# Kernel tuning notes

Hardware: AMD Instinct MI355X
Metric: run time of the kernel (lower is better)

The kernel has to match this reference:

```python
import jax, jax.numpy as jnp
import numpy as np
from jax import lax

VOCAB, EMB, HID = 50000, 1024, 1024
H2 = HID // 2            # per-direction LSTM hidden
T = 4096                 # sequence length
NTAGS, START, STOP = 5, 3, 4
NEG = -10000.0


def setup_inputs() -> dict:
    key = jax.random.key(0)
    ks = jax.random.split(key, 16)
    n = lambda i, shape, s=0.05: (jax.random.normal(ks[i], shape) * s).astype(jnp.float32)
    inp = {
        "sentence": jax.random.randint(ks[0], (T,), 0, VOCAB, dtype=jnp.int64 if jax.config.jax_enable_x64 else jnp.int32),
        "h0": jax.random.normal(ks[1], (2, H2), jnp.float32),
        "c0": jax.random.normal(ks[2], (2, H2), jnp.float32),
        "embed": jax.random.normal(ks[3], (VOCAB, EMB), jnp.float32),
        "Wih_f": n(4, (4 * H2, EMB)), "Whh_f": n(5, (4 * H2, H2)),
        "bih_f": n(6, (4 * H2,)),     "bhh_f": n(7, (4 * H2,)),
        "Wih_b": n(8, (4 * H2, EMB)), "Whh_b": n(9, (4 * H2, H2)),
        "bih_b": n(10, (4 * H2,)),    "bhh_b": n(11, (4 * H2,)),
        "Wout": n(12, (NTAGS, HID)),  "bout": n(13, (NTAGS,)),
    }
    trans = jax.random.normal(ks[14], (NTAGS, NTAGS), jnp.float32)
    trans = trans.at[START, :].set(NEG).at[:, STOP].set(NEG)
    inp["trans"] = trans
    return inp


def _lstm_dir(xs, h0, c0, Wih, Whh, bih, bhh):
    # torch LSTM gate order: i, f, g, o
    def step(carry, x):
        h, c = carry
        g = Wih @ x + bih + Whh @ h + bhh
        i, f, gg, o = jnp.split(g, 4)
        c = jax.nn.sigmoid(f) * c + jax.nn.sigmoid(i) * jnp.tanh(gg)
        h = jax.nn.sigmoid(o) * jnp.tanh(c)
        return (h, c), h
    _, hs = lax.scan(step, (h0, c0), xs)
    return hs  # [T, H2]


def reference(sentence, h0, c0, embed,
              Wih_f, Whh_f, bih_f, bhh_f,
              Wih_b, Whh_b, bih_b, bhh_b,
              Wout, bout, trans):
    xs = embed[sentence]  # [T, EMB]
    hf = _lstm_dir(xs, h0[0], c0[0], Wih_f, Whh_f, bih_f, bhh_f)
    hb = _lstm_dir(xs[::-1], h0[1], c0[1], Wih_b, Whh_b, bih_b, bhh_b)[::-1]
    feats = jnp.concatenate([hf, hb], axis=-1) @ Wout.T + bout  # [T, NTAGS]

    # Viterbi decode
    fv0 = jnp.full((NTAGS,), NEG, jnp.float32).at[START].set(0.0)

    def vstep(fv, feat):
        scores = fv[None, :] + trans            # [next_tag, prev_tag]
        bp = jnp.argmax(scores, axis=1)         # best prev for each next
        fv_new = jnp.max(scores, axis=1) + feat
        return fv_new, bp

    fv, bptrs = lax.scan(vstep, fv0, feats)     # bptrs: [T, NTAGS]
    terminal = fv + trans[STOP]
    best = jnp.argmax(terminal)
    path_score = terminal[best]

    def back(tag, bp):
        prev = bp[tag]
        return prev, prev
    _, path_rev = lax.scan(back, best, bptrs[::-1])  # tags at t=T-1..0, last is START
    full = jnp.concatenate([best[None], path_rev])    # length T+1
    best_path = full[::-1][1:]                        # drop START, forward order, length T
    return path_score, best_path
```

## Files before the change

kernel.cpp:

```cpp
#include <hip/hip_runtime.h>
#include <math.h>

#define VOCAB 50000
#define EMB   1024
#define H2    512
#define R4    2048
#define TLEN  4096
#define NTAGS 5
#define STARTT 3
#define STOPT  4
#define NEGV  (-10000.0f)

#define DWG   32
#define SLICE 16

typedef unsigned long long u64;

#define ALOAD64(p)    __hip_atomic_load((p), __ATOMIC_RELAXED, __HIP_MEMORY_SCOPE_AGENT)
#define ASTORE64(p,v) __hip_atomic_store((p), (v), __ATOMIC_RELAXED, __HIP_MEMORY_SCOPE_AGENT)

__device__ __forceinline__ float fsig(float x) {
    return __builtin_amdgcn_rcpf(1.f + __expf(-x));
}
__device__ __forceinline__ float ftanh(float x) {
    return 1.f - 2.f * __builtin_amdgcn_rcpf(1.f + __expf(2.f * x));
}

__global__ __launch_bounds__(256) void input_gemm(
    const int* __restrict__ sent, const float* __restrict__ embed,
    const float* __restrict__ WihF, const float* __restrict__ WihB,
    const float* __restrict__ bihF, const float* __restrict__ bhhF,
    const float* __restrict__ bihB, const float* __restrict__ bhhB,
    float* __restrict__ G)
{
    __shared__ float As[32 * 64];
    __shared__ float Bs[32 * 64];
    const int tid = threadIdx.x;
    const int tm = blockIdx.x * 64;
    const int tn = blockIdx.y * 64;
    const int dir = blockIdx.z;
    const float* Wih = dir ? WihB : WihF;

    const int lr = tid >> 2;
    const int lp = tid & 3;
    const int srow = sent[tm + lr];
    const float* arow = embed + (size_t)srow * EMB;
    const float* brow = Wih + (size_t)(tn + lr) * EMB;

    const int mt = (tid & 15) * 4;
    const int nt = (tid >> 4) * 4;
    float acc[4][4] = {};

    for (int k0 = 0; k0 < EMB; k0 += 32) {
        float4 a0 = *(const float4*)(arow + k0 + lp * 8);
        float4 a1 = *(const float4*)(arow + k0 + lp * 8 + 4);
        float4 b0 = *(const float4*)(brow + k0 + lp * 8);
        float4 b1 = *(const float4*)(brow + k0 + lp * 8 + 4);
        __syncthreads();
        const int kb = lp * 8;
        As[(kb + 0) * 64 + lr] = a0.x; As[(kb + 1) * 64 + lr] = a0.y;
        As[(kb + 2) * 64 + lr] = a0.z; As[(kb + 3) * 64 + lr] = a0.w;
        As[(kb + 4) * 64 + lr] = a1.x; As[(kb + 5) * 64 + lr] = a1.y;
        As[(kb + 6) * 64 + lr] = a1.z; As[(kb + 7) * 64 + lr] = a1.w;
        Bs[(kb + 0) * 64 + lr] = b0.x; Bs[(kb + 1) * 64 + lr] = b0.y;
        Bs[(kb + 2) * 64 + lr] = b0.z; Bs[(kb + 3) * 64 + lr] = b0.w;
        Bs[(kb + 4) * 64 + lr] = b1.x; Bs[(kb + 5) * 64 + lr] = b1.y;
        Bs[(kb + 6) * 64 + lr] = b1.z; Bs[(kb + 7) * 64 + lr] = b1.w;
        __syncthreads();
        #pragma unroll
        for (int k = 0; k < 32; ++k) {
            float4 av = *(const float4*)(As + k * 64 + mt);
            float4 bv = *(const float4*)(Bs + k * 64 + nt);
            acc[0][0] += av.x * bv.x; acc[0][1] += av.x * bv.y; acc[0][2] += av.x * bv.z; acc[0][3] += av.x * bv.w;
            acc[1][0] += av.y * bv.x; acc[1][1] += av.y * bv.y; acc[1][2] += av.y * bv.z; acc[1][3] += av.y * bv.w;
            acc[2][0] += av.z * bv.x; acc[2][1] += av.z * bv.y; acc[2][2] += av.z * bv.z; acc[2][3] += av.z * bv.w;
            acc[3][0] += av.w * bv.x; acc[3][1] += av.w * bv.y; acc[3][2] += av.w * bv.z; acc[3][3] += av.w * bv.w;
        }
    }

    const float* bih = dir ? bihB : bihF;
    const float* bhh = dir ? bhhB : bhhF;
    float4 bias;
    bias.x = bih[tn + nt + 0] + bhh[tn + nt + 0];
    bias.y = bih[tn + nt + 1] + bhh[tn + nt + 1];
    bias.z = bih[tn + nt + 2] + bhh[tn + nt + 2];
    bias.w = bih[tn + nt + 3] + bhh[tn + nt + 3];
    float* Gd = G + (size_t)dir * TLEN * R4;
    #pragma unroll
    for (int ii = 0; ii < 4; ++ii) {
        float4 o;
        o.x = acc[ii][0] + bias.x; o.y = acc[ii][1] + bias.y;
        o.z = acc[ii][2] + bias.z; o.w = acc[ii][3] + bias.w;
        *(float4*)(Gd + (size_t)(tm + mt + ii) * R4 + tn + nt) = o;
    }
}

__global__ __launch_bounds__(256, 1) void lstm_rec(
    const float* __restrict__ WhhF, const float* __restrict__ WhhB,
    const float* __restrict__ h0, const float* __restrict__ c0,
    const float* __restrict__ G, float* __restrict__ hs,
    u64* hbuf)
{
    const int tid  = threadIdx.x;
    const int dir  = blockIdx.x >> 5;
    const int wg   = blockIdx.x & 31;
    const int base = wg * SLICE;
    const int wave = tid >> 6;
    const int wl   = tid & 63;
    const int e_loc = wl >> 4;
    const int gp    = (wl >> 3) & 1;
    const int qs    = wl & 7;
    const int e     = wave * 4 + e_loc;
    const int grow0 = gp * H2 + base + e;
    const int grow1 = (gp + 2) * H2 + base + e;
    const bool prod = (wl & 15) == 0;
    const float* Whh = dir ? WhhB : WhhF;

    float4 W0[16], W1[16];
    {
        const float4* s0 = (const float4*)(Whh + (size_t)grow0 * H2 + qs * 64);
        const float4* s1 = (const float4*)(Whh + (size_t)grow1 * H2 + qs * 64);
        #pragma unroll
        for (int j = 0; j < 16; ++j) { W0[j] = s0[j]; W1[j] = s1[j]; }
    }

    __shared__ float hsh[8 * 68];

    u64* hb = hbuf + (size_t)dir * 2 * H2;
    float cc = 0.f;
    if (prod) {
        cc = c0[dir * H2 + base + e];
        float hv = h0[dir * H2 + base + e];
        u64 pack = ((u64)1u << 32) | (u64)__float_as_uint(hv);
        ASTORE64(hb + base + e, pack);
    }

    const float* Gd = G + (size_t)dir * TLEN * R4;
    float* hsd = hs + (size_t)dir * TLEN * H2;

    for (int s = 0; s < TLEN; ++s) {
        const int t = dir ? (TLEN - 1 - s) : s;
        const float* gptr = Gd + (size_t)t * R4;
        float gva = gptr[grow0];
        float gvb = gptr[grow1];

        const unsigned want = (unsigned)(s + 1);
        u64* src = hb + (s & 1) * H2 + tid * 2;
        u64 v0 = ALOAD64(src);
        u64 v1 = ALOAD64(src + 1);
        while ((unsigned)(v0 >> 32) != want || (unsigned)(v1 >> 32) != want) {
            v0 = ALOAD64(src);
            v1 = ALOAD64(src + 1);
        }

        {
            int i0 = tid * 2;
            int seg = i0 >> 6, idx = i0 & 63;
            hsh[seg * 68 + idx]     = __uint_as_float((unsigned)v0);
            hsh[seg * 68 + idx + 1] = __uint_as_float((unsigned)v1);
        }
        __syncthreads();

        const float4* hq = (const float4*)(hsh + qs * 68);
        float p00 = 0.f, p01 = 0.f, p02 = 0.f, p03 = 0.f;
        float p10 = 0.f, p11 = 0.f, p12 = 0.f, p13 = 0.f;
        #pragma unroll
        for (int j = 0; j < 16; ++j) {
            float4 h4 = hq[j];
            p00 += W0[j].x * h4.x; p01 += W0[j].y * h4.y;
            p02 += W0[j].z * h4.z; p03 += W0[j].w * h4.w;
            p10 += W1[j].x * h4.x; p11 += W1[j].y * h4.y;
            p12 += W1[j].z * h4.z; p13 += W1[j].w * h4.w;
        }
        float t0 = (p00 + p01) + (p02 + p03);
        float t1 = (p10 + p11) + (p12 + p13);
        t0 += __shfl_xor(t0, 1); t0 += __shfl_xor(t0, 2); t0 += __shfl_xor(t0, 4);
        t1 += __shfl_xor(t1, 1); t1 += __shfl_xor(t1, 2); t1 += __shfl_xor(t1, 4);
        t0 += gva;
        t1 += gvb;

        const int lb = wl & 48;
        float pf = __shfl(t0, lb + 8);
        float po = __shfl(t1, lb + 8);

        if (prod) {
            float i_ = fsig(t0);
            float f_ = fsig(pf);
            float g_ = ftanh(t1);
            float o_ = fsig(po);
            cc = f_ * cc + i_ * g_;
            float hn = o_ * ftanh(cc);
            u64 pack = ((u64)(unsigned)(s + 2) << 32) | (u64)__float_as_uint(hn);
            ASTORE64(hb + ((s + 1) & 1) * H2 + base + e, pack);
            hsd[(size_t)t * H2 + base + e] = hn;
        }
        __syncthreads();
    }
}

__global__ __launch_bounds__(64) void feat_kernel(
    const float* __restrict__ hs, const float* __restrict__ Wout,
    const float* __restrict__ bout, float* __restrict__ feats)
{
    const int t = blockIdx.x;
    const int lane = threadIdx.x;
    const float* hf = hs + (size_t)t * H2;
    const float* hb = hs + (size_t)TLEN * H2 + (size_t)t * H2;
    float x[16];
    #pragma unroll
    for (int r = 0; r < 8; ++r) x[r] = hf[lane + r * 64];
    #pragma unroll
    for (int r = 0; r < 8; ++r) x[8 + r] = hb[lane + r * 64];
    for (int j = 0; j < NTAGS; ++j) {
        const float* wr = Wout + (size_t)j * EMB;
        float p = 0.f;
        #pragma unroll
        for (int r = 0; r < 8; ++r) p += x[r] * wr[lane + r * 64];
        #pragma unroll
        for (int r = 0; r < 8; ++r) p += x[8 + r] * wr[H2 + lane + r * 64];
        #pragma unroll
        for (int off = 32; off > 0; off >>= 1) p += __shfl_down(p, off);
        if (lane == 0) feats[t * NTAGS + j] = p + bout[j];
    }
}

__global__ __launch_bounds__(64) void viterbi_kernel(
    const float* __restrict__ feats, const float* __restrict__ trans,
    float* __restrict__ out)
{
    __shared__ unsigned bp[TLEN];
    __shared__ float fch[256 * NTAGS];
    const int lane = threadIdx.x;
    const bool act = lane < 25;
    const int j = act ? (lane / 5) : 0;
    const int i = act ? (lane % 5) : 0;
    const int j5 = j * 5;
    const float tji = act ? trans[j * 5 + i] : -1e30f;
    float fv = (i == STARTT) ? 0.f : NEGV;

    for (int c0 = 0; c0 < TLEN; c0 += 256) {
        __syncthreads();
        for (int m = lane; m < 256 * NTAGS; m += 64) fch[m] = feats[c0 * NTAGS + m];
        __syncthreads();
        for (int tt = 0; tt < 256; ++tt) {
            float score = fv + tji;
            float v0 = __shfl(score, j5 + 0);
            float v1 = __shfl(score, j5 + 1);
            float v2 = __shfl(score, j5 + 2);
            float v3 = __shfl(score, j5 + 3);
            float v4 = __shfl(score, j5 + 4);
            float mm = v0; int mi = 0;
            if (v1 > mm) { mm = v1; mi = 1; }
            if (v2 > mm) { mm = v2; mi = 2; }
            if (v3 > mm) { mm = v3; mi = 3; }
            if (v4 > mm) { mm = v4; mi = 4; }
            float fnew = mm + fch[tt * NTAGS + j];
            unsigned word = ((unsigned)__shfl(mi, 0)  & 7u)
                          | (((unsigned)__shfl(mi, 5)  & 7u) << 3)
                          | (((unsigned)__shfl(mi, 10) & 7u) << 6)
                          | (((unsigned)__shfl(mi, 15) & 7u) << 9)
                          | (((unsigned)__shfl(mi, 20) & 7u) << 12);
            if (lane == 0) bp[c0 + tt] = word;
            fv = __shfl(fnew, i * 5);
        }
    }
    __syncthreads();

    float tstop = (lane < 5) ? trans[STOPT * 5 + lane] : -1e30f;
    float term = fv + tstop;
    float b0 = __shfl(term, 0), b1 = __shfl(term, 1), b2 = __shfl(term, 2);
    float b3 = __shfl(term, 3), b4 = __shfl(term, 4);
    float bsc = b0; int best = 0;
    if (b1 > bsc) { bsc = b1; best = 1; }
    if (b2 > bsc) { bsc = b2; best = 2; }
    if (b3 > bsc) { bsc = b3; best = 3; }
    if (b4 > bsc) { bsc = b4; best = 4; }

    if (lane == 0) {
        out[0] = bsc;
        int tag = best;
        out[TLEN] = (float)tag;
        #pragma unroll 16
        for (int t = TLEN - 1; t >= 1; --t) {
            tag = (int)((bp[t] >> (3 * tag)) & 7u);
            out[t] = (float)tag;
        }
    }
}

extern "C" void kernel_launch(void* const* d_in, const int* in_sizes, int n_in,
                              void* d_out, int out_size, void* d_ws, size_t ws_size,
                              hipStream_t stream) {
    const int*   sent  = (const int*)d_in[0];
    const float* h0    = (const float*)d_in[1];
    const float* c0    = (const float*)d_in[2];
    const float* embed = (const float*)d_in[3];
    const float* Wih_f = (const float*)d_in[4];
    const float* Whh_f = (const float*)d_in[5];
    const float* bih_f = (const float*)d_in[6];
    const float* bhh_f = (const float*)d_in[7];
    const float* Wih_b = (const float*)d_in[8];
    const float* Whh_b = (const float*)d_in[9];
    const float* bih_b = (const float*)d_in[10];
    const float* bhh_b = (const float*)d_in[11];
    const float* Wout  = (const float*)d_in[12];
    const float* bout  = (const float*)d_in[13];
    const float* trans = (const float*)d_in[14];

    char* ws = (char*)d_ws;
    float*    G     = (float*)(ws);
    float*    hs    = (float*)(ws + 67108864);
    u64*      hbuf  = (u64*)(ws + 83886080);
    float*    feats = (float*)(ws + 83918848);

    input_gemm<<<dim3(TLEN / 64, R4 / 64, 2), 256, 0, stream>>>(
        sent, embed, Wih_f, Wih_b, bih_f, bhh_f, bih_b, bhh_b, G);
    lstm_rec<<<2 * DWG, 256, 0, stream>>>(Whh_f, Whh_b, h0, c0, G, hs, hbuf);
    feat_kernel<<<TLEN, 64, 0, stream>>>(hs, Wout, bout, feats);
    viterbi_kernel<<<1, 64, 0, stream>>>(feats, trans, (float*)d_out);
}
```

Baseline: 8.535 ms.

## Interleave both LSTM directions per workgroup with fp16 dot2 weights and prefetch

The recurrent kernel now runs on 32 workgroups, each handling both directions in alternating phases, so one direction's spin-wait on the other workgroups overlaps the other direction's compute. Recurrent weights are held in registers as fp16 pairs and multiplied with fdot2 against fp16-converted hidden state, with DPP-based reductions in place of shuffles. The input GEMM writes gates interleaved per hidden unit so each step loads one float4 of gate preactivations, which is prefetched for the next step. Costs: fp16 rounding of weights and hidden state can change Viterbi argmax decisions, and the GEMM epilogue now does scattered scalar stores.

```diff
diff --git a/kernel.cpp b/kernel.cpp
--- a/kernel.cpp
+++ b/kernel.cpp
@@ -11,10 +11,11 @@
 #define STOPT  4
 #define NEGV  (-10000.0f)
 
-#define DWG   32
+#define NWG   32
 #define SLICE 16
 
 typedef unsigned long long u64;
+typedef _Float16 half2v __attribute__((ext_vector_type(2)));
 
 #define ALOAD64(p)    __hip_atomic_load((p), __ATOMIC_RELAXED, __HIP_MEMORY_SCOPE_AGENT)
 #define ASTORE64(p,v) __hip_atomic_store((p), (v), __ATOMIC_RELAXED, __HIP_MEMORY_SCOPE_AGENT)
@@ -25,6 +26,18 @@
 __device__ __forceinline__ float ftanh(float x) {
     return 1.f - 2.f * __builtin_amdgcn_rcpf(1.f + __expf(2.f * x));
 }
+
+template <int CTRL>
+__device__ __forceinline__ float dppadd(float x) {
+    int o = __builtin_amdgcn_update_dpp(0, __float_as_int(x), CTRL, 0xf, 0xf, true);
+    return x + __int_as_float(o);
+}
+#define RED16(a) do { \
+    a = dppadd<0xB1>(a);    \
+    a = dppadd<0x4E>(a);    \
+    a = dppadd<0x141>(a);   \
+    a = dppadd<0x128>(a);   \
+} while (0)
 
 __global__ __launch_bounds__(256) void input_gemm(
     const int* __restrict__ sent, const float* __restrict__ embed,
@@ -80,18 +93,19 @@
 
     const float* bih = dir ? bihB : bihF;
     const float* bhh = dir ? bhhB : bhhF;
-    float4 bias;
-    bias.x = bih[tn + nt + 0] + bhh[tn + nt + 0];
-    bias.y = bih[tn + nt + 1] + bhh[tn + nt + 1];
-    bias.z = bih[tn + nt + 2] + bhh[tn + nt + 2];
-    bias.w = bih[tn + nt + 3] + bhh[tn + nt + 3];
+    float bias[4];
+    #pragma unroll
+    for (int jj = 0; jj < 4; ++jj)
+        bias[jj] = bih[tn + nt + jj] + bhh[tn + nt + jj];
     float* Gd = G + (size_t)dir * TLEN * R4;
     #pragma unroll
     for (int ii = 0; ii < 4; ++ii) {
-        float4 o;
-        o.x = acc[ii][0] + bias.x; o.y = acc[ii][1] + bias.y;
-        o.z = acc[ii][2] + bias.z; o.w = acc[ii][3] + bias.w;
-        *(float4*)(Gd + (size_t)(tm + mt + ii) * R4 + tn + nt) = o;
+        #pragma unroll
+        for (int jj = 0; jj < 4; ++jj) {
+            int n = tn + nt + jj;
+            int gate = n >> 9, ee = n & 511;
+            Gd[(size_t)(tm + mt + ii) * R4 + ee * 4 + gate] = acc[ii][jj] + bias[jj];
+        }
     }
 }
 
@@ -102,100 +116,138 @@
     u64* hbuf)
 {
     const int tid  = threadIdx.x;
-    const int dir  = blockIdx.x >> 5;
-    const int wg   = blockIdx.x & 31;
-    const int base = wg * SLICE;
+    const int base = blockIdx.x * SLICE;
     const int wave = tid >> 6;
     const int wl   = tid & 63;
     const int e_loc = wl >> 4;
-    const int gp    = (wl >> 3) & 1;
-    const int qs    = wl & 7;
+    const int seg   = wl & 15;
     const int e     = wave * 4 + e_loc;
-    const int grow0 = gp * H2 + base + e;
-    const int grow1 = (gp + 2) * H2 + base + e;
-    const bool prod = (wl & 15) == 0;
-    const float* Whh = dir ? WhhB : WhhF;
-
-    float4 W0[16], W1[16];
-    {
-        const float4* s0 = (const float4*)(Whh + (size_t)grow0 * H2 + qs * 64);
-        const float4* s1 = (const float4*)(Whh + (size_t)grow1 * H2 + qs * 64);
-        #pragma unroll
-        for (int j = 0; j < 16; ++j) { W0[j] = s0[j]; W1[j] = s1[j]; }
-    }
-
-    __shared__ float hsh[8 * 68];
-
-    u64* hb = hbuf + (size_t)dir * 2 * H2;
-    float cc = 0.f;
+    const bool prod = (seg == 0);
+
+    half2v WA[4][16], WB[4][16];
+    #pragma unroll
+    for (int g = 0; g < 4; ++g) {
+        const float* sa = WhhF + (size_t)(g * H2 + base + e) * H2 + seg * 32;
+        const float* sb = WhhB + (size_t)(g * H2 + base + e) * H2 + seg * 32;
+        #pragma unroll
+        for (int k = 0; k < 16; ++k) {
+            half2v wa, wb;
+            wa[0] = (_Float16)sa[2 * k]; wa[1] = (_Float16)sa[2 * k + 1];
+            wb[0] = (_Float16)sb[2 * k]; wb[1] = (_Float16)sb[2 * k + 1];
+            WA[g][k] = wa; WB[g][k] = wb;
+        }
+    }
+
+    __shared__ __align__(16) unsigned hstg[2][16 * 20 + 8];
+
+    u64* hb0 = hbuf;
+    u64* hb1 = hbuf + 2 * H2;
+    const int slot = tid * 2;
+    const int spos = (tid >> 4) * 20 + (tid & 15);
+
+    float cc0 = 0.f, cc1 = 0.f;
     if (prod) {
-        cc = c0[dir * H2 + base + e];
-        float hv = h0[dir * H2 + base + e];
-        u64 pack = ((u64)1u << 32) | (u64)__float_as_uint(hv);
-        ASTORE64(hb + base + e, pack);
-    }
-
-    const float* Gd = G + (size_t)dir * TLEN * R4;
-    float* hsd = hs + (size_t)dir * TLEN * H2;
+        cc0 = c0[0 * H2 + base + e];
+        cc1 = c0[1 * H2 + base + e];
+        ASTORE64(hb0 + base + e, ((u64)1u << 32) | __float_as_uint(h0[0 * H2 + base + e]));
+        ASTORE64(hb1 + base + e, ((u64)1u << 32) | __float_as_uint(h0[1 * H2 + base + e]));
+    }
+
+    const float* G0 = G;
+    const float* G1 = G + (size_t)TLEN * R4;
+    float* hs0 = hs;
+    float* hs1 = hs + (size_t)TLEN * H2;
+
+    u64 p0a = ALOAD64(hb0 + slot), p0b = ALOAD64(hb0 + slot + 1);
+    float4 gA = *(const float4*)(G0 + (base + e) * 4);
+    float4 gB = *(const float4*)(G1 + (size_t)(TLEN - 1) * R4 + (base + e) * 4);
+
+    #define DOT16(WARR, DBUF, A0, A1, A2, A3) do {                          \
+        const uint4* Hr = (const uint4*)&hstg[DBUF][seg * 20];              \
+        uint4 q0 = Hr[0], q1 = Hr[1], q2 = Hr[2], q3 = Hr[3];               \
+        unsigned xs[16] = {q0.x,q0.y,q0.z,q0.w, q1.x,q1.y,q1.z,q1.w,        \
+                           q2.x,q2.y,q2.z,q2.w, q3.x,q3.y,q3.z,q3.w};       \
+        _Pragma("unroll")                                                   \
+        for (int k = 0; k < 16; ++k) {                                      \
+            half2v x = __builtin_bit_cast(half2v, xs[k]);                   \
+            A0 = __builtin_amdgcn_fdot2(WARR[0][k], x, A0, false);          \
+            A1 = __builtin_amdgcn_fdot2(WARR[1][k], x, A1, false);          \
+            A2 = __builtin_amdgcn_fdot2(WARR[2][k], x, A2, false);          \
+            A3 = __builtin_amdgcn_fdot2(WARR[3][k], x, A3, false);          \
+        } } while (0)
 
     for (int s = 0; s < TLEN; ++s) {
-        const int t = dir ? (TLEN - 1 - s) : s;
-        const float* gptr = Gd + (size_t)t * R4;
-        float gva = gptr[grow0];
-        float gvb = gptr[grow1];
-
         const unsigned want = (unsigned)(s + 1);
-        u64* src = hb + (s & 1) * H2 + tid * 2;
-        u64 v0 = ALOAD64(src);
-        u64 v1 = ALOAD64(src + 1);
-        while ((unsigned)(v0 >> 32) != want || (unsigned)(v1 >> 32) != want) {
-            v0 = ALOAD64(src);
-            v1 = ALOAD64(src + 1);
-        }
-
+        const int rp = s & 1, wp = (s + 1) & 1;
+        const int snx = (s + 1 < TLEN) ? s + 1 : s;
+
+        while ((unsigned)(p0a >> 32) != want || (unsigned)(p0b >> 32) != want) {
+            p0a = ALOAD64(hb0 + rp * H2 + slot);
+            p0b = ALOAD64(hb0 + rp * H2 + slot + 1);
+        }
         {
-            int i0 = tid * 2;
-            int seg = i0 >> 6, idx = i0 & 63;
-            hsh[seg * 68 + idx]     = __uint_as_float((unsigned)v0);
-            hsh[seg * 68 + idx + 1] = __uint_as_float((unsigned)v1);
-        }
-        __syncthreads();
-
-        const float4* hq = (const float4*)(hsh + qs * 68);
-        float p00 = 0.f, p01 = 0.f, p02 = 0.f, p03 = 0.f;
-        float p10 = 0.f, p11 = 0.f, p12 = 0.f, p13 = 0.f;
-        #pragma unroll
-        for (int j = 0; j < 16; ++j) {
-            float4 h4 = hq[j];
-            p00 += W0[j].x * h4.x; p01 += W0[j].y * h4.y;
-            p02 += W0[j].z * h4.z; p03 += W0[j].w * h4.w;
-            p10 += W1[j].x * h4.x; p11 += W1[j].y * h4.y;
-            p12 += W1[j].z * h4.z; p13 += W1[j].w * h4.w;
-        }
-        float t0 = (p00 + p01) + (p02 + p03);
-        float t1 = (p10 + p11) + (p12 + p13);
-        t0 += __shfl_xor(t0, 1); t0 += __shfl_xor(t0, 2); t0 += __shfl_xor(t0, 4);
-        t1 += __shfl_xor(t1, 1); t1 += __shfl_xor(t1, 2); t1 += __shfl_xor(t1, 4);
-        t0 += gva;
-        t1 += gvb;
-
-        const int lb = wl & 48;
-        float pf = __shfl(t0, lb + 8);
-        float po = __shfl(t1, lb + 8);
+            half2v hp;
+            hp[0] = (_Float16)__uint_as_float((unsigned)p0a);
+            hp[1] = (_Float16)__uint_as_float((unsigned)p0b);
+            hstg[0][spos] = __builtin_bit_cast(unsigned, hp);
+        }
+        __syncthreads();
+
+        u64 p1a = ALOAD64(hb1 + rp * H2 + slot);
+        u64 p1b = ALOAD64(hb1 + rp * H2 + slot + 1);
+        float4 gAn = *(const float4*)(G0 + (size_t)snx * R4 + (base + e) * 4);
+
+        float a0 = 0.f, a1 = 0.f, a2 = 0.f, a3 = 0.f;
+        DOT16(WA, 0, a0, a1, a2, a3);
+        RED16(a0); RED16(a1); RED16(a2); RED16(a3);
 
         if (prod) {
-            float i_ = fsig(t0);
-            float f_ = fsig(pf);
-            float g_ = ftanh(t1);
-            float o_ = fsig(po);
-            cc = f_ * cc + i_ * g_;
-            float hn = o_ * ftanh(cc);
-            u64 pack = ((u64)(unsigned)(s + 2) << 32) | (u64)__float_as_uint(hn);
-            ASTORE64(hb + ((s + 1) & 1) * H2 + base + e, pack);
-            hsd[(size_t)t * H2 + base + e] = hn;
-        }
-        __syncthreads();
-    }
+            float i_ = fsig(a0 + gA.x);
+            float f_ = fsig(a1 + gA.y);
+            float g_ = ftanh(a2 + gA.z);
+            float o_ = fsig(a3 + gA.w);
+            cc0 = f_ * cc0 + i_ * g_;
+            float hn = o_ * ftanh(cc0);
+            ASTORE64(hb0 + wp * H2 + base + e,
+                     ((u64)(unsigned)(s + 2) << 32) | __float_as_uint(hn));
+            hs0[(size_t)s * H2 + base + e] = hn;
+        }
+        gA = gAn;
+
+        while ((unsigned)(p1a >> 32) != want || (unsigned)(p1b >> 32) != want) {
+            p1a = ALOAD64(hb1 + rp * H2 + slot);
+            p1b = ALOAD64(hb1 + rp * H2 + slot + 1);
+        }
+        {
+            half2v hp;
+            hp[0] = (_Float16)__uint_as_float((unsigned)p1a);
+            hp[1] = (_Float16)__uint_as_float((unsigned)p1b);
+            hstg[1][spos] = __builtin_bit_cast(unsigned, hp);
+        }
+        __syncthreads();
+
+        p0a = ALOAD64(hb0 + wp * H2 + slot);
+        p0b = ALOAD64(hb0 + wp * H2 + slot + 1);
+        float4 gBn = *(const float4*)(G1 + (size_t)(TLEN - 1 - snx) * R4 + (base + e) * 4);
+
+        float b0 = 0.f, b1 = 0.f, b2 = 0.f, b3 = 0.f;
+        DOT16(WB, 1, b0, b1, b2, b3);
+        RED16(b0); RED16(b1); RED16(b2); RED16(b3);
+
+        if (prod) {
+            float i_ = fsig(b0 + gB.x);
+            float f_ = fsig(b1 + gB.y);
+            float g_ = ftanh(b2 + gB.z);
+            float o_ = fsig(b3 + gB.w);
+            cc1 = f_ * cc1 + i_ * g_;
+            float hn = o_ * ftanh(cc1);
+            ASTORE64(hb1 + wp * H2 + base + e,
+                     ((u64)(unsigned)(s + 2) << 32) | __float_as_uint(hn));
+            hs1[(size_t)(TLEN - 1 - s) * H2 + base + e] = hn;
+        }
+        gB = gBn;
+    }
+    #undef DOT16
 }
 
 __global__ __launch_bounds__(64) void feat_kernel(
@@ -315,7 +367,7 @@
 
     input_gemm<<<dim3(TLEN / 64, R4 / 64, 2), 256, 0, stream>>>(
         sent, embed, Wih_f, Wih_b, bih_f, bhh_f, bih_b, bhh_b, G);
-    lstm_rec<<<2 * DWG, 256, 0, stream>>>(Whh_f, Whh_b, h0, c0, G, hs, hbuf);
+    lstm_rec<<<NWG, 256, 0, stream>>>(Whh_f, Whh_b, h0, c0, G, hs, hbuf);
     feat_kernel<<<TLEN, 64, 0, stream>>>(hs, Wout, bout, feats);
     viterbi_kernel<<<1, 64, 0, stream>>>(feats, trans, (float*)d_out);
 }
```

Measured after the change: 8.813 ms. 1.03x slower.
